# Kernel optimization log

Measured on AMD Instinct MI355X. Metric: run time of the kernel, lower is better.

The kernel has to match this reference:

```python
import jax, jax.numpy as jnp
import numpy as np

EPS = 1e-5

def _ln(x, g, b):
    m = jnp.mean(x, axis=-1, keepdims=True)
    v = jnp.mean((x - m) ** 2, axis=-1, keepdims=True)
    return (x - m) / jnp.sqrt(v + EPS) * g + b

B, SX, SY = 2, 2048, 2048
XD, YD, P, H, MULT = 1024, 1024, 64, 16, 4

def setup_inputs() -> dict:
    key = jax.random.key(0)
    ks = jax.random.split(key, 20)
    s = lambda fan: 1.0 / np.sqrt(fan)
    return {
        "x": jax.random.normal(ks[0], (B, SX, XD), jnp.float32),
        "y": jax.random.normal(ks[1], (B, SY, YD), jnp.float32),
        "gx_gamma": jnp.ones((XD,), jnp.float32),
        "gx_beta": jnp.zeros((XD,), jnp.float32),
        "gy_gamma": jnp.ones((YD,), jnp.float32),
        "gy_beta": jnp.zeros((YD,), jnp.float32),
        "Wq": jax.random.uniform(ks[2], (H, XD, P), jnp.float32, -s(XD), s(XD)),
        "bq": jax.random.uniform(ks[3], (H, P), jnp.float32, -s(XD), s(XD)),
        "Wk": jax.random.uniform(ks[4], (H, YD, P), jnp.float32, -s(YD), s(YD)),
        "bk": jax.random.uniform(ks[5], (H, P), jnp.float32, -s(YD), s(YD)),
        "Wv": jax.random.uniform(ks[6], (H, YD, P), jnp.float32, -s(YD), s(YD)),
        "bv": jax.random.uniform(ks[7], (H, P), jnp.float32, -s(YD), s(YD)),
        "Wo": jax.random.uniform(ks[8], (H * P, XD), jnp.float32, -s(H * P), s(H * P)),
        "bo": jax.random.uniform(ks[9], (XD,), jnp.float32, -s(H * P), s(H * P)),
        "gd_gamma": jnp.ones((XD,), jnp.float32),
        "gd_beta": jnp.zeros((XD,), jnp.float32),
        "W1": jax.random.uniform(ks[10], (XD, MULT * XD), jnp.float32, -s(XD), s(XD)),
        "b1": jax.random.uniform(ks[11], (MULT * XD,), jnp.float32, -s(XD), s(XD)),
        "W2": jax.random.uniform(ks[12], (MULT * XD, XD), jnp.float32, -s(MULT * XD), s(MULT * XD)),
        "b2": jax.random.uniform(ks[13], (XD,), jnp.float32, -s(MULT * XD), s(MULT * XD)),
        "mask": 1,
    }

def reference(x, y, gx_gamma, gx_beta, gy_gamma, gy_beta, Wq, bq, Wk, bk, Wv, bv,
              Wo, bo, gd_gamma, gd_beta, W1, b1, W2, b2, mask):
    xn = _ln(x, gx_gamma, gx_beta)
    yn = _ln(y, gy_gamma, gy_beta)
    # batched per-head projections: [B,S,D] x [H,D,P] -> [B,H,S,P]
    q = jnp.einsum('bsd,hdp->bhsp', xn, Wq) + bq[None, :, None, :]
    k = jnp.einsum('btd,hdp->bhtp', yn, Wk) + bk[None, :, None, :]
    v = jnp.einsum('btd,hdp->bhtp', yn, Wv) + bv[None, :, None, :]
    scores = jnp.einsum('bhsp,bhtp->bhst', q, k) * (1.0 / jnp.sqrt(jnp.float32(P)))
    attn = jax.nn.softmax(scores, axis=-1)
    if mask:
        # post-softmax strictly-upper-triangular mask (torch.triu diagonal=1)
        tri = jnp.triu(jnp.ones((SX, SY), attn.dtype), k=1)
        attn = attn * tri
    o = jnp.einsum('bhst,bhtp->bhsp', attn, v)          # [B,H,S,P]
    o = o.transpose(0, 2, 1, 3).reshape(B, SX, H * P)    # concat heads
    x2 = x + o @ Wo + bo
    h = jax.nn.gelu(_ln(x2, gd_gamma, gd_beta) @ W1 + b1, approximate=False)
    return x2 + h @ W2 + b2
```

## Files before the change

### kernel.cpp

```cpp
#include <hip/hip_runtime.h>
#include <hip/hip_bf16.h>
#include <math.h>

typedef __bf16 bf16_t;
typedef __bf16 bf16x8 __attribute__((ext_vector_type(8)));
typedef __bf16 bf16x4 __attribute__((ext_vector_type(4)));
typedef float f32x4 __attribute__((ext_vector_type(4)));

#define QSCALE 0.18033688011112042f

static __device__ __forceinline__ f32x4 mfma16(bf16x8 a, bf16x8 b, f32x4 c) {
  return __builtin_amdgcn_mfma_f32_16x16x32_bf16(a, b, c, 0, 0, 0);
}

static __device__ __forceinline__ float gelu_f(float x) {
  return 0.5f * x * (1.0f + erff(x * 0.70710678118654752440f));
}

static __device__ __forceinline__ float exp2_fast(float x) {
  float r;
  asm("v_exp_f32 %0, %1" : "=v"(r) : "v"(x));
  return r;
}

typedef __attribute__((address_space(1))) const void as1_void;
typedef __attribute__((address_space(3))) void as3_void;
static __device__ __forceinline__ void gload16(const void* g, void* s) {
  __builtin_amdgcn_global_load_lds((as1_void*)g, (as3_void*)s, 16, 0, 0);
}

static __device__ __forceinline__ long hmi(int row, int col) {
  return ((((long)(row >> 11) * 16 + (col >> 6)) * 2048) + (row & 2047)) * 64 + (col & 63);
}

__global__ __launch_bounds__(256) void prep_weights(
    const float* __restrict__ Wq, const float* __restrict__ Wk, const float* __restrict__ Wv,
    const float* __restrict__ Wo, const float* __restrict__ W1, const float* __restrict__ W2,
    bf16_t* __restrict__ WqkvT, bf16_t* __restrict__ WoT, bf16_t* __restrict__ W1T,
    bf16_t* __restrict__ W2T) {
  const int bid = blockIdx.x;
  const float* inp;
  bf16_t* outp;
  int istride, ostride, i0, j0;
  if (bid < 768) {
    const int wsel = bid >> 8, rem = bid & 255;
    const int h = rem >> 4, xt = rem & 15;
    const float* W = wsel == 0 ? Wq : (wsel == 1 ? Wk : Wv);
    inp = W + h * 65536;
    outp = WqkvT + (long)wsel * 1048576 + h * 65536;
    istride = 64; ostride = 1024; i0 = xt * 64; j0 = 0;
  } else if (bid < 1024) {
    const int rem = bid - 768;
    inp = Wo; outp = WoT; istride = 1024; ostride = 1024;
    i0 = (rem & 15) * 64; j0 = (rem >> 4) * 64;
  } else if (bid < 2048) {
    const int rem = bid - 1024;
    inp = W1; outp = W1T; istride = 4096; ostride = 1024;
    i0 = (rem & 15) * 64; j0 = (rem >> 4) * 64;
  } else {
    const int rem = bid - 2048;
    inp = W2; outp = W2T; istride = 1024; ostride = 4096;
    i0 = (rem >> 4) * 64; j0 = (rem & 15) * 64;
  }
  __shared__ bf16_t tile[64][65];
  const int r = threadIdx.x >> 2, cs = (threadIdx.x & 3) * 16;
#pragma unroll
  for (int jj = 0; jj < 16; jj++)
    tile[cs + jj][r] = (bf16_t)inp[(long)(i0 + r) * istride + j0 + cs + jj];
  __syncthreads();
#pragma unroll
  for (int jj = 0; jj < 16; jj++)
    outp[(long)(j0 + r) * ostride + i0 + cs + jj] = tile[r][cs + jj];
}

static __device__ __forceinline__ void ln_body(const float* __restrict__ in,
                                               const float* __restrict__ g,
                                               const float* __restrict__ be, int row,
                                               bf16_t* __restrict__ out) {
  const int t = threadIdx.x;
  const float4 xv = ((const float4*)(in + (long)row * 1024))[t];
  float s1 = xv.x + xv.y + xv.z + xv.w;
  float s2 = xv.x * xv.x + xv.y * xv.y + xv.z * xv.z + xv.w * xv.w;
#pragma unroll
  for (int m = 1; m < 64; m <<= 1) {
    s1 += __shfl_xor(s1, m);
    s2 += __shfl_xor(s2, m);
  }
  __shared__ float r1[4], r2[4];
  if ((t & 63) == 0) { r1[t >> 6] = s1; r2[t >> 6] = s2; }
  __syncthreads();
  s1 = r1[0] + r1[1] + r1[2] + r1[3];
  s2 = r2[0] + r2[1] + r2[2] + r2[3];
  const float mean = s1 * (1.0f / 1024.0f);
  float var = s2 * (1.0f / 1024.0f) - mean * mean;
  const float rstd = rsqrtf(fmaxf(var, 0.0f) + 1e-5f);
  const float4 gv = ((const float4*)g)[t];
  const float4 bv = ((const float4*)be)[t];
  bf16x4 o;
  o[0] = (bf16_t)((xv.x - mean) * rstd * gv.x + bv.x);
  o[1] = (bf16_t)((xv.y - mean) * rstd * gv.y + bv.y);
  o[2] = (bf16_t)((xv.z - mean) * rstd * gv.z + bv.z);
  o[3] = (bf16_t)((xv.w - mean) * rstd * gv.w + bv.w);
  *(bf16x4*)(out + (long)row * 1024 + t * 4) = o;
}

__global__ __launch_bounds__(256) void ln_kernel(const float* __restrict__ in,
                                                 const float* __restrict__ g,
                                                 const float* __restrict__ be,
                                                 bf16_t* __restrict__ out) {
  ln_body(in, g, be, blockIdx.x, out);
}

__global__ __launch_bounds__(256) void ln2_kernel(
    const float* __restrict__ x, const float* __restrict__ y, const float* __restrict__ gx,
    const float* __restrict__ bex, const float* __restrict__ gy, const float* __restrict__ bey,
    bf16_t* __restrict__ xn, bf16_t* __restrict__ yn) {
  const int row = blockIdx.x;
  if (row < 4096) ln_body(x, gx, bex, row, xn);
  else ln_body(y, gy, bey, row - 4096, yn);
}

__global__ __launch_bounds__(256) void vtrans_kernel(const bf16_t* __restrict__ vb,
                                                     bf16_t* __restrict__ vTb) {
  const int z = blockIdx.y;
  const bf16_t* ip = vb + ((long)(z >> 4) * 2048) * 1024 + (z & 15) * 64;
  bf16_t* op = vTb + (long)z * 131072;
  const int i0 = blockIdx.x * 64;
  __shared__ bf16_t tile[64][65];
  const int r = threadIdx.x >> 2, cs = (threadIdx.x & 3) * 16;
#pragma unroll
  for (int jj = 0; jj < 16; jj++)
    tile[cs + jj][r] = ip[(long)(i0 + r) * 1024 + cs + jj];
  __syncthreads();
#pragma unroll
  for (int jj = 0; jj < 16; jj++)
    op[(long)r * 2048 + i0 + cs + jj] = tile[r][cs + jj];
}

template <int EPI, int BN>
__global__ __launch_bounds__(256) void gemm_bt(const bf16_t* __restrict__ A,
                                               const bf16_t* __restrict__ A2,
                                               const bf16_t* __restrict__ Bt,
                                               const float* __restrict__ bias,
                                               const float* __restrict__ biasB,
                                               const float* __restrict__ biasC,
                                               const float* __restrict__ res,
                                               void* __restrict__ Cout,
                                               int M, int N, int K) {
  constexpr int NF = BN / 32;
  constexpr int NBI = BN / 32;
  __shared__ bf16_t a_lds[2][128 * 64];
  __shared__ bf16_t b_lds[2][BN * 64];
  const int tid = threadIdx.x, l = tid & 63, w = tid >> 6;
  const int wr = w >> 1, wc = w & 1;
  const int nwg = gridDim.x * gridDim.y;
  const int orig = blockIdx.y * gridDim.x + blockIdx.x;
  const int lid = (orig & 7) * (nwg >> 3) + (orig >> 3);
  const int bx = lid % gridDim.x, by = lid / gridDim.x;
  const int m0 = by * 128, n0 = bx * BN;
  const bf16_t* Ause = (EPI == 5 && n0 >= 1024) ? A2 : A;
  const int lr = l & 15, lg = l >> 4;
  long a_src[4];
  int ldst[4];
#pragma unroll
  for (int i = 0; i < 4; i++) {
    const int row = i * 32 + w * 8 + (l >> 3);
    const int sc = ((l & 7) ^ (row & 7)) * 8;
    a_src[i] = (long)(m0 + row) * K + sc;
    ldst[i] = (i * 32 + w * 8) * 64;
  }
  long b_src[NBI];
#pragma unroll
  for (int i = 0; i < NBI; i++) {
    const int row = i * 32 + w * 8 + (l >> 3);
    const int sc = ((l & 7) ^ (row & 7)) * 8;
    b_src[i] = (long)(n0 + row) * K + sc;
  }
  const int nk = K >> 6;
  f32x4 acc[4][NF] = {};
#pragma unroll
  for (int i = 0; i < 4; i++) gload16(Ause + a_src[i], &a_lds[0][ldst[i]]);
#pragma unroll
  for (int i = 0; i < NBI; i++) gload16(Bt + b_src[i], &b_lds[0][ldst[i]]);
  __syncthreads();
  const int sw = (lr & 7) << 4;
  int cur = 0;
  for (int t = 0; t < nk; t++) {
    if (t + 1 < nk) {
      const long k0 = (long)(t + 1) * 64;
#pragma unroll
      for (int i = 0; i < 4; i++) gload16(Ause + a_src[i] + k0, &a_lds[cur ^ 1][ldst[i]]);
#pragma unroll
      for (int i = 0; i < NBI; i++) gload16(Bt + b_src[i] + k0, &b_lds[cur ^ 1][ldst[i]]);
    }
    const char* ab = (const char*)&a_lds[cur][0];
    const char* bb = (const char*)&b_lds[cur][0];
    bf16x8 af[4][2], bfr[NF][2];
#pragma unroll
    for (int m = 0; m < 4; m++) {
      const int rb = (wr * 64 + m * 16 + lr) * 128;
      af[m][0] = *(const bf16x8*)(ab + rb + ((16 * lg) ^ sw));
      af[m][1] = *(const bf16x8*)(ab + rb + ((16 * lg + 64) ^ sw));
    }
#pragma unroll
    for (int n = 0; n < NF; n++) {
      const int rb = (wc * (BN / 2) + n * 16 + lr) * 128;
      bfr[n][0] = *(const bf16x8*)(bb + rb + ((16 * lg) ^ sw));
      bfr[n][1] = *(const bf16x8*)(bb + rb + ((16 * lg + 64) ^ sw));
    }
    __builtin_amdgcn_s_setprio(1);
#pragma unroll
    for (int kk = 0; kk < 2; kk++)
#pragma unroll
      for (int m = 0; m < 4; m++)
#pragma unroll
        for (int n = 0; n < NF; n++)
          acc[m][n] = mfma16(af[m][kk], bfr[n][kk], acc[m][n]);
    __builtin_amdgcn_s_setprio(0);
    __syncthreads();
    cur ^= 1;
  }
#pragma unroll
  for (int m = 0; m < 4; m++)
#pragma unroll
    for (int n = 0; n < NF; n++) {
      const int row_b = m0 + wr * 64 + m * 16 + (l >> 4) * 4;
      const int col = n0 + wc * (BN / 2) + n * 16 + lr;
#pragma unroll
      for (int r = 0; r < 4; r++) {
        const int row = row_b + r;
        const float v = acc[m][n][r];
        if (EPI == 1) {
          const long idx = (long)row * N + col;
          ((float*)Cout)[idx] = v + bias[col] + res[idx];
        } else if (EPI == 2) {
          const long idx = (long)row * N + col;
          ((bf16_t*)Cout)[idx] = (bf16_t)gelu_f(v + bias[col]);
        } else if (EPI == 5) {
          if (col < 1024) {
            ((bf16_t*)Cout)[hmi(row, col)] = (bf16_t)((v + bias[col]) * QSCALE);
          } else if (col < 2048) {
            ((bf16_t*)Cout + 4194304)[hmi(row, col - 1024)] = (bf16_t)(v + biasB[col - 1024]);
          } else {
            ((bf16_t*)Cout + 8388608)[(long)row * 1024 + (col - 2048)] =
                (bf16_t)(v + biasC[col - 2048]);
          }
        }
      }
    }
}

__global__ __launch_bounds__(256) void attn_kernel(const bf16_t* __restrict__ qhm,
                                                   const bf16_t* __restrict__ khm,
                                                   const bf16_t* __restrict__ vtg,
                                                   bf16_t* __restrict__ og,
                                                   const int* __restrict__ maskp) {
  const int T = 2048, HP = 1024;
  __shared__ bf16_t k_lds[2][64 * 64];
  __shared__ bf16_t vt_lds[2][64 * 64];
  __shared__ bf16_t p_lds[4 * 32 * 72];
  const int bh = blockIdx.x, b = bh >> 4, h = bh & 15;
  const int q0 = blockIdx.y * 128;
  const int tid = threadIdx.x, l = tid & 63, w = tid >> 6;
  const int lr = l & 15, lg = l >> 4, lg4 = lg * 4;
  const int srow0 = q0 + w * 32 + lr;
  const bf16_t* kbase = khm + (long)bh * T * 64;
  const bf16_t* vbase = vtg + (long)bh * 64 * T;
  bf16x8 qf[2][2];
#pragma unroll
  for (int g = 0; g < 2; g++) {
    const bf16_t* qr = qhm + ((long)bh * 2048 + srow0 + g * 16) * 64 + lg * 8;
    qf[g][0] = *(const bf16x8*)qr;
    qf[g][1] = *(const bf16x8*)(qr + 32);
  }
  bf16_t* pl = &p_lds[w * 32 * 72];
  float lpart[2] = {0.0f, 0.0f};
  f32x4 oat[4][2] = {};

  const int swz = (lr & 7) << 4;
  const int fo0 = lr * 128 + ((16 * lg) ^ swz);
  const int fo1 = lr * 128 + ((64 + 16 * lg) ^ swz);

  const bool do_mask = (maskp[0] != 0);
  const int nM = do_mask ? (q0 >> 6) : 0;
  const int nt = T >> 6;

  const int sch = l & 7, srow8 = l >> 3;
  int cur = 0;
  {
    const bool needV = (nM == 0);
#pragma unroll
    for (int i = 0; i < 2; i++) {
      const int row = (i * 4 + w) * 8 + srow8;
      const int sc = (sch ^ (row & 7)) * 8;
      gload16(kbase + (long)row * 64 + sc, &k_lds[0][(i * 4 + w) * 512]);
      if (needV) gload16(vbase + (long)row * 2048 + 0 + sc, &vt_lds[0][(i * 4 + w) * 512]);
    }
  }
  __syncthreads();

  for (int t = 0; t < nt; t++) {
    const int t0 = t << 6;
    const int mode = (t < nM) ? 0 : ((do_mask && t < nM + 2) ? 1 : 2);
    if (t + 1 < nt) {
      const int t1 = (t + 1) << 6;
      const bool needV = (t + 1) >= nM;
#pragma unroll
      for (int i = 0; i < 2; i++) {
        const int row = (i * 4 + w) * 8 + srow8;
        const int sc = (sch ^ (row & 7)) * 8;
        gload16(kbase + (long)(t1 + row) * 64 + sc, &k_lds[cur ^ 1][(i * 4 + w) * 512]);
        if (needV)
          gload16(vbase + (long)row * 2048 + t1 + sc, &vt_lds[cur ^ 1][(i * 4 + w) * 512]);
      }
    }
    const char* kb = (const char*)&k_lds[cur][0];
    f32x4 sacc[4][2];
    __builtin_amdgcn_s_setprio(1);
#pragma unroll
    for (int n = 0; n < 4; n++) {
      bf16x8 kf0 = *(const bf16x8*)(kb + n * 2048 + fo0);
      bf16x8 kf1 = *(const bf16x8*)(kb + n * 2048 + fo1);
#pragma unroll
      for (int g = 0; g < 2; g++) {
        f32x4 z = {0.0f, 0.0f, 0.0f, 0.0f};
        z = mfma16(kf0, qf[g][0], z);
        sacc[n][g] = mfma16(kf1, qf[g][1], z);
      }
    }
    __builtin_amdgcn_s_setprio(0);
    float pv[2][4][4];
#pragma unroll
    for (int g = 0; g < 2; g++) {
      float psn[4];
#pragma unroll
      for (int n = 0; n < 4; n++) {
        pv[g][n][0] = exp2_fast(sacc[n][g][0]);
        pv[g][n][1] = exp2_fast(sacc[n][g][1]);
        pv[g][n][2] = exp2_fast(sacc[n][g][2]);
        pv[g][n][3] = exp2_fast(sacc[n][g][3]);
        psn[n] = (pv[g][n][0] + pv[g][n][1]) + (pv[g][n][2] + pv[g][n][3]);
      }
      lpart[g] += (psn[0] + psn[1]) + (psn[2] + psn[3]);
    }
    if (mode > 0) {
#pragma unroll
      for (int g = 0; g < 2; g++)
#pragma unroll
        for (int n = 0; n < 4; n++) {
          bf16x4 pk;
#pragma unroll
          for (int r = 0; r < 4; r++) {
            float v = pv[g][n][r];
            if (mode == 1 && (t0 + n * 16 + lg4 + r) <= srow0 + g * 16) v = 0.0f;
            pk[r] = (bf16_t)v;
          }
          *(bf16x4*)&pl[(g * 16 + lr) * 72 + n * 16 + lg4] = pk;
        }
      const char* vtb = (const char*)&vt_lds[cur][0];
      __builtin_amdgcn_s_setprio(1);
#pragma unroll
      for (int kk = 0; kk < 2; kk++) {
        bf16x8 pb0 = *(bf16x8*)&pl[lr * 72 + kk * 32 + lg * 8];
        bf16x8 pb1 = *(bf16x8*)&pl[(16 + lr) * 72 + kk * 32 + lg * 8];
        const int fkk = lr * 128 + ((kk * 64 + 16 * lg) ^ swz);
#pragma unroll
        for (int np = 0; np < 4; np++) {
          bf16x8 vtf = *(const bf16x8*)(vtb + np * 2048 + fkk);
          oat[np][0] = mfma16(vtf, pb0, oat[np][0]);
          oat[np][1] = mfma16(vtf, pb1, oat[np][1]);
        }
      }
      __builtin_amdgcn_s_setprio(0);
    }
    __syncthreads();
    cur ^= 1;
  }
  float inv[2];
#pragma unroll
  for (int g = 0; g < 2; g++) {
    float lsum = lpart[g];
    lsum += __shfl_xor(lsum, 16);
    lsum += __shfl_xor(lsum, 32);
    inv[g] = 1.0f / lsum;
  }
#pragma unroll
  for (int g = 0; g < 2; g++)
#pragma unroll
    for (int np = 0; np < 4; np++) {
      bf16x4 o4;
#pragma unroll
      for (int r = 0; r < 4; r++) o4[r] = (bf16_t)(oat[np][g][r] * inv[g]);
      *(bf16x4*)&pl[(g * 16 + lr) * 72 + np * 16 + lg4] = o4;
    }
  const int es = l >> 2, ec = (l & 3) * 16;
#pragma unroll
  for (int g = 0; g < 2; g++) {
    bf16x8 o0 = *(bf16x8*)&pl[(g * 16 + es) * 72 + ec];
    bf16x8 o1 = *(bf16x8*)&pl[(g * 16 + es) * 72 + ec + 8];
    bf16_t* orow = og + (long)(b * 2048 + q0 + w * 32 + g * 16 + es) * HP + h * 64 + ec;
    *(bf16x8*)&orow[0] = o0;
    *(bf16x8*)&orow[8] = o1;
  }
}

extern "C" void kernel_launch(void* const* d_in, const int* in_sizes, int n_in,
                              void* d_out, int out_size, void* d_ws, size_t ws_size,
                              hipStream_t stream) {
  const float* x = (const float*)d_in[0];
  const float* y = (const float*)d_in[1];
  const float* gxg = (const float*)d_in[2];
  const float* gxb = (const float*)d_in[3];
  const float* gyg = (const float*)d_in[4];
  const float* gyb = (const float*)d_in[5];
  const float* Wq = (const float*)d_in[6];
  const float* bq = (const float*)d_in[7];
  const float* Wk = (const float*)d_in[8];
  const float* bk = (const float*)d_in[9];
  const float* Wv = (const float*)d_in[10];
  const float* bv = (const float*)d_in[11];
  const float* Wo = (const float*)d_in[12];
  const float* bo = (const float*)d_in[13];
  const float* gdg = (const float*)d_in[14];
  const float* gdb = (const float*)d_in[15];
  const float* W1 = (const float*)d_in[16];
  const float* b1 = (const float*)d_in[17];
  const float* W2 = (const float*)d_in[18];
  const float* b2 = (const float*)d_in[19];
  const int* maskp = (const int*)d_in[20];
  float* out = (float*)d_out;

  char* ws = (char*)d_ws;
  const long MB = 1024 * 1024;
  bf16_t* xn = (bf16_t*)(ws + 0);
  bf16_t* yn = (bf16_t*)(ws + 8 * MB);
  bf16_t* WqkvT = (bf16_t*)(ws + 16 * MB);
  bf16_t* WoT = (bf16_t*)(ws + 22 * MB);
  bf16_t* W1T = (bf16_t*)(ws + 24 * MB);
  bf16_t* W2T = (bf16_t*)(ws + 32 * MB);
  bf16_t* qhm = (bf16_t*)(ws + 40 * MB);
  bf16_t* vb = (bf16_t*)(ws + 56 * MB);
  bf16_t* vTb = (bf16_t*)(ws + 64 * MB);
  bf16_t* ob = (bf16_t*)(ws + 0);
  bf16_t* xd = (bf16_t*)(ws + 8 * MB);
  bf16_t* hb = (bf16_t*)(ws + 40 * MB);
  bf16_t* khm = qhm + 4194304;

  prep_weights<<<3072, 256, 0, stream>>>(Wq, Wk, Wv, Wo, W1, W2, WqkvT, WoT, W1T, W2T);
  ln2_kernel<<<8192, 256, 0, stream>>>(x, y, gxg, gxb, gyg, gyb, xn, yn);
  gemm_bt<5, 128><<<dim3(24, 32), 256, 0, stream>>>(xn, yn, WqkvT, bq, bk, bv, nullptr, qhm,
                                                    4096, 3072, 1024);
  vtrans_kernel<<<dim3(32, 32), 256, 0, stream>>>(vb, vTb);
  attn_kernel<<<dim3(32, 16), 256, 0, stream>>>(qhm, khm, vTb, ob, maskp);
  gemm_bt<1, 64><<<dim3(16, 32), 256, 0, stream>>>(ob, nullptr, WoT, bo, nullptr, nullptr, x,
                                                   out, 4096, 1024, 1024);
  ln_kernel<<<4096, 256, 0, stream>>>(out, gdg, gdb, xd);
  gemm_bt<2, 128><<<dim3(32, 32), 256, 0, stream>>>(xd, nullptr, W1T, b1, nullptr, nullptr,
                                                    nullptr, hb, 4096, 4096, 1024);
  gemm_bt<1, 64><<<dim3(16, 32), 256, 0, stream>>>(hb, nullptr, W2T, b2, nullptr, nullptr, out,
                                                   out, 4096, 1024, 4096);
}
```

Measured before the change: 272.2 us.

## Merge weight prep with LayerNorm, fuse V transpose into QKV GEMM epilogue, add K32 GEMM

```diff
diff --git a/kernel.cpp b/kernel.cpp
--- a/kernel.cpp
+++ b/kernel.cpp
@@ -33,12 +33,48 @@
   return ((((long)(row >> 11) * 16 + (col >> 6)) * 2048) + (row & 2047)) * 64 + (col & 63);
 }
 
-__global__ __launch_bounds__(256) void prep_weights(
+__global__ __launch_bounds__(256) void prep_all(
     const float* __restrict__ Wq, const float* __restrict__ Wk, const float* __restrict__ Wv,
     const float* __restrict__ Wo, const float* __restrict__ W1, const float* __restrict__ W2,
     bf16_t* __restrict__ WqkvT, bf16_t* __restrict__ WoT, bf16_t* __restrict__ W1T,
-    bf16_t* __restrict__ W2T) {
+    bf16_t* __restrict__ W2T, const float* __restrict__ x, const float* __restrict__ y,
+    const float* __restrict__ gx, const float* __restrict__ bex, const float* __restrict__ gy,
+    const float* __restrict__ bey, bf16_t* __restrict__ xn, bf16_t* __restrict__ yn) {
   const int bid = blockIdx.x;
+  if (bid >= 3072) {
+    const int lrow = bid - 3072;
+    const float* in = lrow < 4096 ? x : y;
+    const float* g = lrow < 4096 ? gx : gy;
+    const float* be = lrow < 4096 ? bex : bey;
+    bf16_t* out = lrow < 4096 ? xn : yn;
+    const int row = lrow & 4095;
+    const int t = threadIdx.x;
+    const float4 xv = ((const float4*)(in + (long)row * 1024))[t];
+    float s1 = xv.x + xv.y + xv.z + xv.w;
+    float s2 = xv.x * xv.x + xv.y * xv.y + xv.z * xv.z + xv.w * xv.w;
+#pragma unroll
+    for (int m = 1; m < 64; m <<= 1) {
+      s1 += __shfl_xor(s1, m);
+      s2 += __shfl_xor(s2, m);
+    }
+    __shared__ float r1[4], r2[4];
+    if ((t & 63) == 0) { r1[t >> 6] = s1; r2[t >> 6] = s2; }
+    __syncthreads();
+    s1 = r1[0] + r1[1] + r1[2] + r1[3];
+    s2 = r2[0] + r2[1] + r2[2] + r2[3];
+    const float mean = s1 * (1.0f / 1024.0f);
+    float var = s2 * (1.0f / 1024.0f) - mean * mean;
+    const float rstd = rsqrtf(fmaxf(var, 0.0f) + 1e-5f);
+    const float4 gv = ((const float4*)g)[t];
+    const float4 bv = ((const float4*)be)[t];
+    bf16x4 o;
+    o[0] = (bf16_t)((xv.x - mean) * rstd * gv.x + bv.x);
+    o[1] = (bf16_t)((xv.y - mean) * rstd * gv.y + bv.y);
+    o[2] = (bf16_t)((xv.z - mean) * rstd * gv.z + bv.z);
+    o[3] = (bf16_t)((xv.w - mean) * rstd * gv.w + bv.w);
+    *(bf16x4*)(out + (long)row * 1024 + t * 4) = o;
+    return;
+  }
   const float* inp;
   bf16_t* outp;
   int istride, ostride, i0, j0;
@@ -73,11 +109,11 @@
     outp[(long)(j0 + r) * ostride + i0 + cs + jj] = tile[r][cs + jj];
 }
 
-static __device__ __forceinline__ void ln_body(const float* __restrict__ in,
-                                               const float* __restrict__ g,
-                                               const float* __restrict__ be, int row,
-                                               bf16_t* __restrict__ out) {
-  const int t = threadIdx.x;
+__global__ __launch_bounds__(256) void ln_kernel(const float* __restrict__ in,
+                                                 const float* __restrict__ g,
+                                                 const float* __restrict__ be,
+                                                 bf16_t* __restrict__ out) {
+  const int row = blockIdx.x, t = threadIdx.x;
   const float4 xv = ((const float4*)(in + (long)row * 1024))[t];
   float s1 = xv.x + xv.y + xv.z + xv.w;
   float s2 = xv.x * xv.x + xv.y * xv.y + xv.z * xv.z + xv.w * xv.w;
@@ -104,49 +140,128 @@
   *(bf16x4*)(out + (long)row * 1024 + t * 4) = o;
 }
 
-__global__ __launch_bounds__(256) void ln_kernel(const float* __restrict__ in,
-                                                 const float* __restrict__ g,
-                                                 const float* __restrict__ be,
-                                                 bf16_t* __restrict__ out) {
-  ln_body(in, g, be, blockIdx.x, out);
-}
-
-__global__ __launch_bounds__(256) void ln2_kernel(
-    const float* __restrict__ x, const float* __restrict__ y, const float* __restrict__ gx,
-    const float* __restrict__ bex, const float* __restrict__ gy, const float* __restrict__ bey,
-    bf16_t* __restrict__ xn, bf16_t* __restrict__ yn) {
-  const int row = blockIdx.x;
-  if (row < 4096) ln_body(x, gx, bex, row, xn);
-  else ln_body(y, gy, bey, row - 4096, yn);
-}
-
-__global__ __launch_bounds__(256) void vtrans_kernel(const bf16_t* __restrict__ vb,
-                                                     bf16_t* __restrict__ vTb) {
-  const int z = blockIdx.y;
-  const bf16_t* ip = vb + ((long)(z >> 4) * 2048) * 1024 + (z & 15) * 64;
-  bf16_t* op = vTb + (long)z * 131072;
-  const int i0 = blockIdx.x * 64;
-  __shared__ bf16_t tile[64][65];
-  const int r = threadIdx.x >> 2, cs = (threadIdx.x & 3) * 16;
-#pragma unroll
-  for (int jj = 0; jj < 16; jj++)
-    tile[cs + jj][r] = ip[(long)(i0 + r) * 1024 + cs + jj];
+template <int EPI, int BN>
+__global__ __launch_bounds__(256) void gemm32(const bf16_t* __restrict__ A,
+                                              const bf16_t* __restrict__ A2,
+                                              const bf16_t* __restrict__ Bt,
+                                              const float* __restrict__ bias,
+                                              const float* __restrict__ biasB,
+                                              const float* __restrict__ biasC,
+                                              bf16_t* __restrict__ aux,
+                                              void* __restrict__ Cout,
+                                              int M, int N, int K) {
+  constexpr int NF = BN / 32;
+  constexpr int NBI = BN / 64;
+  __shared__ bf16_t a_lds[2][128 * 32];
+  __shared__ bf16_t b_lds[2][BN * 32];
+  const int tid = threadIdx.x, l = tid & 63, w = tid >> 6;
+  const int wr = w >> 1, wc = w & 1;
+  const int nwg = gridDim.x * gridDim.y;
+  const int orig = blockIdx.y * gridDim.x + blockIdx.x;
+  const int lid = (orig & 7) * (nwg >> 3) + (orig >> 3);
+  const int bx = lid % gridDim.x, by = lid / gridDim.x;
+  const int m0 = by * 128, n0 = bx * BN;
+  const bf16_t* Ause = (EPI == 5 && n0 >= 1024) ? A2 : A;
+  const int lr = l & 15, lg = l >> 4;
+  long a_src[2];
+  int a_dst[2];
+#pragma unroll
+  for (int i = 0; i < 2; i++) {
+    const int row = i * 64 + (tid >> 2);
+    const int sc = ((tid & 3) ^ (row & 3)) * 8;
+    a_src[i] = (long)(m0 + row) * K + sc;
+    a_dst[i] = (i * 64 + w * 16) * 32;
+  }
+  long b_src[NBI];
+#pragma unroll
+  for (int i = 0; i < NBI; i++) {
+    const int row = i * 64 + (tid >> 2);
+    const int sc = ((tid & 3) ^ (row & 3)) * 8;
+    b_src[i] = (long)(n0 + row) * K + sc;
+  }
+  const int nk = K >> 5;
+  f32x4 acc[4][NF] = {};
+#pragma unroll
+  for (int i = 0; i < 2; i++) gload16(Ause + a_src[i], &a_lds[0][a_dst[i]]);
+#pragma unroll
+  for (int i = 0; i < NBI; i++) gload16(Bt + b_src[i], &b_lds[0][a_dst[i]]);
   __syncthreads();
-#pragma unroll
-  for (int jj = 0; jj < 16; jj++)
-    op[(long)r * 2048 + i0 + cs + jj] = tile[r][cs + jj];
+  int cur = 0;
+  for (int t = 0; t < nk; t++) {
+    if (t + 1 < nk) {
+      const long k0 = (long)(t + 1) * 32;
+#pragma unroll
+      for (int i = 0; i < 2; i++) gload16(Ause + a_src[i] + k0, &a_lds[cur ^ 1][a_dst[i]]);
+#pragma unroll
+      for (int i = 0; i < NBI; i++) gload16(Bt + b_src[i] + k0, &b_lds[cur ^ 1][a_dst[i]]);
+    }
+    const char* ab = (const char*)&a_lds[cur][0];
+    const char* bb = (const char*)&b_lds[cur][0];
+    bf16x8 af[4], bfr[NF];
+#pragma unroll
+    for (int m = 0; m < 4; m++) {
+      const int row = wr * 64 + m * 16 + lr;
+      af[m] = *(const bf16x8*)(ab + row * 64 + 16 * (lg ^ (row & 3)));
+    }
+#pragma unroll
+    for (int n = 0; n < NF; n++) {
+      const int row = wc * (BN / 2) + n * 16 + lr;
+      bfr[n] = *(const bf16x8*)(bb + row * 64 + 16 * (lg ^ (row & 3)));
+    }
+    __builtin_amdgcn_s_setprio(1);
+#pragma unroll
+    for (int m = 0; m < 4; m++)
+#pragma unroll
+      for (int n = 0; n < NF; n++) acc[m][n] = mfma16(af[m], bfr[n], acc[m][n]);
+    __builtin_amdgcn_s_setprio(0);
+    __syncthreads();
+    cur ^= 1;
+  }
+#pragma unroll
+  for (int m = 0; m < 4; m++)
+#pragma unroll
+    for (int n = 0; n < NF; n++) {
+      const int row_b = m0 + wr * 64 + m * 16 + (l >> 4) * 4;
+      const int col = n0 + wc * (BN / 2) + n * 16 + lr;
+      if (EPI == 2) {
+        const float bia = bias[col];
+#pragma unroll
+        for (int r = 0; r < 4; r++) {
+          const long idx = (long)(row_b + r) * N + col;
+          ((bf16_t*)Cout)[idx] = (bf16_t)gelu_f(acc[m][n][r] + bia);
+        }
+      } else if (EPI == 5) {
+        if (col < 1024) {
+          const float bia = bias[col];
+#pragma unroll
+          for (int r = 0; r < 4; r++)
+            ((bf16_t*)Cout)[hmi(row_b + r, col)] = (bf16_t)((acc[m][n][r] + bia) * QSCALE);
+        } else if (col < 2048) {
+          const float bia = biasB[col - 1024];
+#pragma unroll
+          for (int r = 0; r < 4; r++)
+            ((bf16_t*)Cout + 4194304)[hmi(row_b + r, col - 1024)] =
+                (bf16_t)(acc[m][n][r] + bia);
+        } else {
+          const int vcol = col - 2048;
+          const float bia = biasC[vcol];
+          bf16x4 vv;
+#pragma unroll
+          for (int r = 0; r < 4; r++) vv[r] = (bf16_t)(acc[m][n][r] + bia);
+          const int bb2 = row_b >> 11, tt = row_b & 2047;
+          *(bf16x4*)&aux[(((long)(bb2 << 4) + (vcol >> 6)) * 64 + (vcol & 63)) * 2048 + tt] = vv;
+        }
+      }
+    }
 }
 
 template <int EPI, int BN>
-__global__ __launch_bounds__(256) void gemm_bt(const bf16_t* __restrict__ A,
-                                               const bf16_t* __restrict__ A2,
-                                               const bf16_t* __restrict__ Bt,
-                                               const float* __restrict__ bias,
-                                               const float* __restrict__ biasB,
-                                               const float* __restrict__ biasC,
-                                               const float* __restrict__ res,
-                                               void* __restrict__ Cout,
-                                               int M, int N, int K) {
+__global__ __launch_bounds__(256) void gemm64(const bf16_t* __restrict__ A,
+                                              const bf16_t* __restrict__ Bt,
+                                              const float* __restrict__ bias,
+                                              const float* __restrict__ res,
+                                              void* __restrict__ Cout,
+                                              int M, int N, int K) {
   constexpr int NF = BN / 32;
   constexpr int NBI = BN / 32;
   __shared__ bf16_t a_lds[2][128 * 64];
@@ -158,7 +273,6 @@
   const int lid = (orig & 7) * (nwg >> 3) + (orig >> 3);
   const int bx = lid % gridDim.x, by = lid / gridDim.x;
   const int m0 = by * 128, n0 = bx * BN;
-  const bf16_t* Ause = (EPI == 5 && n0 >= 1024) ? A2 : A;
   const int lr = l & 15, lg = l >> 4;
   long a_src[4];
   int ldst[4];
@@ -179,7 +293,7 @@
   const int nk = K >> 6;
   f32x4 acc[4][NF] = {};
 #pragma unroll
-  for (int i = 0; i < 4; i++) gload16(Ause + a_src[i], &a_lds[0][ldst[i]]);
+  for (int i = 0; i < 4; i++) gload16(A + a_src[i], &a_lds[0][ldst[i]]);
 #pragma unroll
   for (int i = 0; i < NBI; i++) gload16(Bt + b_src[i], &b_lds[0][ldst[i]]);
   __syncthreads();
@@ -189,7 +303,7 @@
     if (t + 1 < nk) {
       const long k0 = (long)(t + 1) * 64;
 #pragma unroll
-      for (int i = 0; i < 4; i++) gload16(Ause + a_src[i] + k0, &a_lds[cur ^ 1][ldst[i]]);
+      for (int i = 0; i < 4; i++) gload16(A + a_src[i] + k0, &a_lds[cur ^ 1][ldst[i]]);
 #pragma unroll
       for (int i = 0; i < NBI; i++) gload16(Bt + b_src[i] + k0, &b_lds[cur ^ 1][ldst[i]]);
     }
@@ -226,26 +340,11 @@
     for (int n = 0; n < NF; n++) {
       const int row_b = m0 + wr * 64 + m * 16 + (l >> 4) * 4;
       const int col = n0 + wc * (BN / 2) + n * 16 + lr;
+      const float bia = bias[col];
 #pragma unroll
       for (int r = 0; r < 4; r++) {
-        const int row = row_b + r;
-        const float v = acc[m][n][r];
-        if (EPI == 1) {
-          const long idx = (long)row * N + col;
-          ((float*)Cout)[idx] = v + bias[col] + res[idx];
-        } else if (EPI == 2) {
-          const long idx = (long)row * N + col;
-          ((bf16_t*)Cout)[idx] = (bf16_t)gelu_f(v + bias[col]);
-        } else if (EPI == 5) {
-          if (col < 1024) {
-            ((bf16_t*)Cout)[hmi(row, col)] = (bf16_t)((v + bias[col]) * QSCALE);
-          } else if (col < 2048) {
-            ((bf16_t*)Cout + 4194304)[hmi(row, col - 1024)] = (bf16_t)(v + biasB[col - 1024]);
-          } else {
-            ((bf16_t*)Cout + 8388608)[(long)row * 1024 + (col - 2048)] =
-                (bf16_t)(v + biasC[col - 2048]);
-          }
-        }
+        const long idx = (long)(row_b + r) * N + col;
+        ((float*)Cout)[idx] = acc[m][n][r] + bia + res[idx];
       }
     }
 }
@@ -439,24 +538,20 @@
   bf16_t* W1T = (bf16_t*)(ws + 24 * MB);
   bf16_t* W2T = (bf16_t*)(ws + 32 * MB);
   bf16_t* qhm = (bf16_t*)(ws + 40 * MB);
-  bf16_t* vb = (bf16_t*)(ws + 56 * MB);
   bf16_t* vTb = (bf16_t*)(ws + 64 * MB);
   bf16_t* ob = (bf16_t*)(ws + 0);
   bf16_t* xd = (bf16_t*)(ws + 8 * MB);
   bf16_t* hb = (bf16_t*)(ws + 40 * MB);
   bf16_t* khm = qhm + 4194304;
 
-  prep_weights<<<3072, 256, 0, stream>>>(Wq, Wk, Wv, Wo, W1, W2, WqkvT, WoT, W1T, W2T);
-  ln2_kernel<<<8192, 256, 0, stream>>>(x, y, gxg, gxb, gyg, gyb, xn, yn);
-  gemm_bt<5, 128><<<dim3(24, 32), 256, 0, stream>>>(xn, yn, WqkvT, bq, bk, bv, nullptr, qhm,
-                                                    4096, 3072, 1024);
-  vtrans_kernel<<<dim3(32, 32), 256, 0, stream>>>(vb, vTb);
+  prep_all<<<11264, 256, 0, stream>>>(Wq, Wk, Wv, Wo, W1, W2, WqkvT, WoT, W1T, W2T, x, y, gxg,
+                                      gxb, gyg, gyb, xn, yn);
+  gemm32<5, 128><<<dim3(24, 32), 256, 0, stream>>>(xn, yn, WqkvT, bq, bk, bv, vTb, qhm, 4096,
+                                                   3072, 1024);
   attn_kernel<<<dim3(32, 16), 256, 0, stream>>>(qhm, khm, vTb, ob, maskp);
-  gemm_bt<1, 64><<<dim3(16, 32), 256, 0, stream>>>(ob, nullptr, WoT, bo, nullptr, nullptr, x,
-                                                   out, 4096, 1024, 1024);
+  gemm64<1, 64><<<dim3(16, 32), 256, 0, stream>>>(ob, WoT, bo, x, out, 4096, 1024, 1024);
   ln_kernel<<<4096, 256, 0, stream>>>(out, gdg, gdb, xd);
-  gemm_bt<2, 128><<<dim3(32, 32), 256, 0, stream>>>(xd, nullptr, W1T, b1, nullptr, nullptr,
-                                                    nullptr, hb, 4096, 4096, 1024);
-  gemm_bt<1, 64><<<dim3(16, 32), 256, 0, stream>>>(hb, nullptr, W2T, b2, nullptr, nullptr, out,
-                                                   out, 4096, 1024, 4096);
-}
+  gemm32<2, 128><<<dim3(32, 32), 256, 0, stream>>>(xd, nullptr, W1T, b1, nullptr, nullptr,
+                                                   nullptr, hb, 4096, 4096, 1024);
+  gemm64<1, 64><<<dim3(16, 32), 256, 0, stream>>>(hb, W2T, b2, out, out, 4096, 1024, 4096);
+}
```

Result: faster. 252.3 us (-7.3%).
